# Kernel tuning notes

Measured on AMD Instinct MI355X. Metric: run time of the kernel, lower is better.

## Reference

```python
import jax, jax.numpy as jnp
import numpy as np

B, Z, TDIM, CF, A, R, T = 1024, 256, 512, 1024, 64, 128, 64

def _lstm_cell(x, h, c, Wih, Whh, b):
    # PyTorch gate order: i, f, g, o
    g = x @ Wih.T + h @ Whh.T + b
    i, f, gg, o = jnp.split(g, 4, axis=-1)
    c = jax.nn.sigmoid(f) * c + jax.nn.sigmoid(i) * jnp.tanh(gg)
    h = jax.nn.sigmoid(o) * jnp.tanh(c)
    return h, c

def setup_inputs() -> dict:
    key = jax.random.key(0)
    ks = jax.random.split(key, 24)
    s = lambda k, shape, fan: jax.random.normal(k, shape, jnp.float32) * (1.0 / np.sqrt(fan))
    d = {}
    d['z'] = jax.random.normal(ks[0], (B, Z), jnp.float32)
    d['z2t_w'] = s(ks[1], (TDIM, Z), Z)
    d['z2t_b'] = jnp.zeros((TDIM,), jnp.float32)
    in_a, in_r, in_t = TDIM + A, TDIM + A + R, TDIM + A + 1
    d['Wih_a'] = s(ks[2], (4 * CF, in_a), in_a); d['Whh_a'] = s(ks[3], (4 * CF, CF), CF); d['b_a'] = jnp.zeros((4 * CF,), jnp.float32)
    d['Wih_r'] = s(ks[4], (4 * CF, in_r), in_r); d['Whh_r'] = s(ks[5], (4 * CF, CF), CF); d['b_r'] = jnp.zeros((4 * CF,), jnp.float32)
    d['Wih_t'] = s(ks[6], (4 * CF, in_t), in_t); d['Whh_t'] = s(ks[7], (4 * CF, CF), CF); d['b_t'] = jnp.zeros((4 * CF,), jnp.float32)
    d['e2act_w'] = s(ks[8], (A, CF), CF); d['e2act_b'] = jnp.zeros((A,), jnp.float32)
    d['e2res_w'] = s(ks[9], (R, CF), CF); d['e2res_b'] = jnp.zeros((R,), jnp.float32)
    d['e2ts_w1'] = s(ks[10], (CF // 2, CF), CF); d['e2ts_b1'] = jnp.zeros((CF // 2,), jnp.float32)
    d['e2ts_w2'] = s(ks[11], (1, CF // 2), CF // 2); d['e2ts_b2'] = jnp.zeros((1,), jnp.float32)
    return d

def reference(z, z2t_w, z2t_b, Wih_a, Whh_a, b_a, Wih_r, Whh_r, b_r, Wih_t, Whh_t, b_t,
              e2act_w, e2act_b, e2res_w, e2res_b, e2ts_w1, e2ts_b1, e2ts_w2, e2ts_b2):
    t_rec = jax.nn.relu(z @ z2t_w.T + z2t_b)                  # [B, TDIM]
    b = t_rec.shape[0]
    act_oh = jnp.tile(jax.nn.one_hot(A - 1, A, dtype=jnp.float32), (b, 1))   # EOT activity
    res_oh = jnp.tile(jax.nn.one_hot(R - 1, R, dtype=jnp.float32), (b, 1))   # EOT resource
    ts_v = jnp.zeros((b, 1), jnp.float32)
    zeros_h = jnp.zeros((b, CF), jnp.float32)
    carry0 = (act_oh, res_oh, ts_v, zeros_h, zeros_h, zeros_h, zeros_h, zeros_h, zeros_h)

    def step(carry, _):
        act_oh, res_oh, ts_v, ha, ca, hr, cr, ht, ct = carry
        xa = jnp.concatenate([t_rec, act_oh], axis=-1)
        ha, ca = _lstm_cell(xa, ha, ca, Wih_a, Whh_a, b_a)
        act_logits = ha @ e2act_w.T + e2act_b                 # [B, A]
        act_oh2 = jax.nn.one_hot(jnp.argmax(act_logits, axis=-1), A, dtype=jnp.float32)
        xr = jnp.concatenate([t_rec, act_oh2, res_oh], axis=-1)
        hr, cr = _lstm_cell(xr, hr, cr, Wih_r, Whh_r, b_r)
        res_logits = hr @ e2res_w.T + e2res_b                 # [B, R]
        res_oh2 = jax.nn.one_hot(jnp.argmax(res_logits, axis=-1), R, dtype=jnp.float32)
        xt = jnp.concatenate([t_rec, act_oh2, ts_v], axis=-1)
        ht, ct = _lstm_cell(xt, ht, ct, Wih_t, Whh_t, b_t)
        ts_new = jax.nn.relu(ht @ e2ts_w1.T + e2ts_b1) @ e2ts_w2.T + e2ts_b2  # [B, 1]
        new_carry = (act_oh2, res_oh2, ts_new, ha, ca, hr, cr, ht, ct)
        return new_carry, (act_logits, res_logits, ts_new)

    _, (act_seq, res_seq, ts_seq) = jax.lax.scan(step, carry0, None, length=T)
    acts_rec = jax.nn.softmax(jnp.transpose(act_seq, (1, 0, 2)), axis=2)   # [B, T, A]
    ress_rec = jax.nn.softmax(jnp.transpose(res_seq, (1, 0, 2)), axis=2)   # [B, T, R]
    ts_rec = jnp.transpose(ts_seq[..., 0], (1, 0))                         # [B, T]
    return acts_rec, ts_rec, ress_rec
```

## Files before the change

kernel.cpp:

```cpp
#include <hip/hip_runtime.h>
#include <math.h>


__device__ __forceinline__ float sigf(float x) { return 1.0f / (1.0f + expf(-x)); }

typedef __attribute__((ext_vector_type(8))) _Float16 f16x8;
typedef __attribute__((ext_vector_type(4))) float f32x4;

__device__ __forceinline__ void split_f16(float x, unsigned short& hi, unsigned short& lo) {
    _Float16 h = (_Float16)x;
    float r = (x - (float)h) * 2048.0f;
    _Float16 l = (_Float16)r;
    hi = __builtin_bit_cast(unsigned short, h);
    lo = __builtin_bit_cast(unsigned short, l);
}

#define GLDS(gp, lp) __builtin_amdgcn_global_load_lds( \
    (const __attribute__((address_space(1))) void*)(gp), \
    (__attribute__((address_space(3))) void*)(lp), 16, 0, 0)

__global__ __launch_bounds__(256) void step1(
    const unsigned short* __restrict__ Ah, const unsigned short* __restrict__ Al,
    const unsigned short* __restrict__ WA0, const unsigned short* __restrict__ WA1,
    const float* __restrict__ base_a, const float* __restrict__ Ea, const int* __restrict__ aidx,
    float* __restrict__ ca, unsigned short* __restrict__ oAh, unsigned short* __restrict__ oAl,
    float* __restrict__ haf,
    const unsigned short* __restrict__ Th, const unsigned short* __restrict__ Tl,
    const unsigned short* __restrict__ W10, const unsigned short* __restrict__ W11,
    const float* __restrict__ b1, float* __restrict__ u,
    const float* __restrict__ hrf, const float* __restrict__ resT4, const float* __restrict__ resb,
    float* __restrict__ out_res, int* __restrict__ ridx, int t, int Loff)
{
    int L = blockIdx.x + Loff;
    if (L >= 576) {
        if (t == 0) return;
        int lane = threadIdx.x & 63, w = threadIdx.x >> 6;
        int b = (L - 576) * 4 + w;
        float acc0 = resb[lane], acc1 = resb[lane + 64];
        const float4* arow = (const float4*)(hrf + (size_t)b * 1024);
#pragma unroll 4
        for (int k4 = 0; k4 < 256; k4++) {
            float4 a4 = arow[k4];
            float4 w40 = *(const float4*)(resT4 + ((size_t)k4 * 128 + lane) * 4);
            float4 w41 = *(const float4*)(resT4 + ((size_t)k4 * 128 + lane + 64) * 4);
            acc0 += a4.x * w40.x + a4.y * w40.y + a4.z * w40.z + a4.w * w40.w;
            acc1 += a4.x * w41.x + a4.y * w41.y + a4.z * w41.z + a4.w * w41.w;
        }
        float v = acc0; int idx = lane;
        if (acc1 > v) { v = acc1; idx = lane + 64; }
#pragma unroll
        for (int off = 32; off; off >>= 1) {
            float ov = __shfl_xor(v, off);
            int   oi = __shfl_xor(idx, off);
            if (ov > v || (ov == v && oi < idx)) { v = ov; idx = oi; }
        }
        float e0 = expf(acc0 - v), e1 = expf(acc1 - v);
        float s = e0 + e1;
#pragma unroll
        for (int off = 32; off; off >>= 1) s += __shfl_xor(s, off);
        float* dst = out_res + ((size_t)b * 64 + (t - 1)) * 128;
        dst[lane] = e0 / s; dst[lane + 64] = e1 / s;
        if (lane == 0) ridx[b] = idx;
        return;
    }

    __shared__ unsigned short lds[24576];
    const unsigned short *pAh, *pAl, *pWh, *pWl;
    int x, jy; bool isA;
    if (L < 512) {
        isA = true;
        int xcd = L & 7, idx = L >> 3;
        jy = xcd * 8 + (idx >> 3);
        x = idx & 7;
        pAh = Ah; pAl = Al; pWh = WA0; pWl = WA1;
    } else {
        isA = false;
        int t2 = L - 512;
        x = t2 & 7; jy = t2 >> 3;
        pAh = Th; pAl = Tl; pWh = W10; pWl = W11;
    }
    const int tid = threadIdx.x, wave = tid >> 6, lane = tid & 63;
    const int lrow = lane & 15, lq = lane >> 4;
    const int m0 = x * 128;

    f32x4 acch[2][4], accl[2][4];
#pragma unroll
    for (int i = 0; i < 2; i++)
#pragma unroll
        for (int j = 0; j < 4; j++) {
            acch[i][j] = (f32x4){0.f, 0.f, 0.f, 0.f};
            accl[i][j] = (f32x4){0.f, 0.f, 0.f, 0.f};
        }

    for (int k0 = 0; k0 < 1024; k0 += 64) {
        __syncthreads();
#pragma unroll
        for (int ss = 0; ss < 2; ss++) {
            int s = wave * 2 + ss;
            int mrow = m0 + s * 16 + lrow;
            int nrow = isA ? (wave * 1024 + jy * 16 + lrow) : (jy * 64 + wave * 16 + lrow);
#pragma unroll
            for (int kh = 0; kh < 2; kh++) {
                int k = k0 + kh * 32 + lq * 8;
                GLDS(pAh + (size_t)mrow * 1024 + k, &lds[s * 1024 + kh * 512]);
                GLDS(pAl + (size_t)mrow * 1024 + k, &lds[8192 + s * 1024 + kh * 512]);
                if (ss == 0) {
                    GLDS(pWh + (size_t)nrow * 1024 + k, &lds[16384 + wave * 1024 + kh * 512]);
                    GLDS(pWl + (size_t)nrow * 1024 + k, &lds[20480 + wave * 1024 + kh * 512]);
                }
            }
        }
        __syncthreads();
#pragma unroll
        for (int kh = 0; kh < 2; kh++) {
            f16x8 ah[2], al[2], bh[4], bl[4];
#pragma unroll
            for (int mi = 0; mi < 2; mi++) {
                ah[mi] = *(const f16x8*)&lds[(wave * 2 + mi) * 1024 + kh * 512 + lane * 8];
                al[mi] = *(const f16x8*)&lds[8192 + (wave * 2 + mi) * 1024 + kh * 512 + lane * 8];
            }
#pragma unroll
            for (int ni = 0; ni < 4; ni++) {
                bh[ni] = *(const f16x8*)&lds[16384 + ni * 1024 + kh * 512 + lane * 8];
                bl[ni] = *(const f16x8*)&lds[20480 + ni * 1024 + kh * 512 + lane * 8];
            }
#pragma unroll
            for (int mi = 0; mi < 2; mi++)
#pragma unroll
                for (int ni = 0; ni < 4; ni++) {
                    acch[mi][ni] = __builtin_amdgcn_mfma_f32_16x16x32_f16(ah[mi], bh[ni], acch[mi][ni], 0, 0, 0);
                    accl[mi][ni] = __builtin_amdgcn_mfma_f32_16x16x32_f16(al[mi], bh[ni], accl[mi][ni], 0, 0, 0);
                    accl[mi][ni] = __builtin_amdgcn_mfma_f32_16x16x32_f16(ah[mi], bl[ni], accl[mi][ni], 0, 0, 0);
                }
        }
    }

    const float s_lo = 1.0f / 2048.0f;
    if (isA) {
        int j = jy * 16 + lrow;
#pragma unroll
        for (int mi = 0; mi < 2; mi++)
#pragma unroll
            for (int r = 0; r < 4; r++) {
                int row = m0 + wave * 32 + mi * 16 + lq * 4 + r;
                size_t rb = (size_t)row * 4096 + j;
                const float* e1 = Ea + (size_t)aidx[row] * 4096 + j;
                float gi = acch[mi][0][r] + accl[mi][0][r] * s_lo + base_a[rb]        + e1[0];
                float gf = acch[mi][1][r] + accl[mi][1][r] * s_lo + base_a[rb + 1024] + e1[1024];
                float gg = acch[mi][2][r] + accl[mi][2][r] * s_lo + base_a[rb + 2048] + e1[2048];
                float go = acch[mi][3][r] + accl[mi][3][r] * s_lo + base_a[rb + 3072] + e1[3072];
                size_t ci = (size_t)row * 1024 + j;
                float cn = sigf(gf) * ca[ci] + sigf(gi) * tanhf(gg);
                ca[ci] = cn;
                float hn = sigf(go) * tanhf(cn);
                haf[ci] = hn;
                split_f16(hn, oAh[ci], oAl[ci]);
            }
    } else {
#pragma unroll
        for (int mi = 0; mi < 2; mi++)
#pragma unroll
            for (int ni = 0; ni < 4; ni++) {
                int col = jy * 64 + ni * 16 + lrow;
                float bv = b1[col];
#pragma unroll
                for (int r = 0; r < 4; r++) {
                    int row = m0 + wave * 32 + mi * 16 + lq * 4 + r;
                    float v = acch[mi][ni][r] + accl[mi][ni][r] * s_lo + bv;
                    u[(size_t)row * 512 + col] = fmaxf(v, 0.0f);
                }
            }
    }
}

__global__ __launch_bounds__(256) void step3(
    const unsigned short* __restrict__ Rh, const unsigned short* __restrict__ Rl,
    const unsigned short* __restrict__ WR0, const unsigned short* __restrict__ WR1,
    const float* __restrict__ base_r, const float* __restrict__ Er_a, const float* __restrict__ Er_r,
    const int* __restrict__ aidx, const int* __restrict__ ridx, const float* __restrict__ tsv,
    float* __restrict__ cr, unsigned short* __restrict__ oRh, unsigned short* __restrict__ oRl,
    float* __restrict__ hrf,
    const unsigned short* __restrict__ Th, const unsigned short* __restrict__ Tl,
    const unsigned short* __restrict__ WT0, const unsigned short* __restrict__ WT1,
    const float* __restrict__ base_t, const float* __restrict__ Et_a, const float* __restrict__ wtts,
    float* __restrict__ ct, unsigned short* __restrict__ oTh, unsigned short* __restrict__ oTl)
{
    __shared__ unsigned short lds[32768];
    int L = blockIdx.x;
    int xcd = L & 7, idx = L >> 3;
    int g = xcd * 8 + (idx >> 3);
    int x = idx & 7;
    int z = g >> 5, y = g & 31;
    const unsigned short* pAh = z ? Th : Rh;
    const unsigned short* pAl = z ? Tl : Rl;
    const unsigned short* pWh = z ? WT0 : WR0;
    const unsigned short* pWl = z ? WT1 : WR1;

    const int tid = threadIdx.x, wave = tid >> 6, lane = tid & 63;
    const int wm = wave >> 1, wn = wave & 1;
    const int lrow = lane & 15, lq = lane >> 4;
    const int m0 = x * 128, j0 = y * 32;

    f32x4 acch[4][4], accl[4][4];
#pragma unroll
    for (int i = 0; i < 4; i++)
#pragma unroll
        for (int j = 0; j < 4; j++) {
            acch[i][j] = (f32x4){0.f, 0.f, 0.f, 0.f};
            accl[i][j] = (f32x4){0.f, 0.f, 0.f, 0.f};
        }

    for (int k0 = 0; k0 < 1024; k0 += 64) {
        __syncthreads();
#pragma unroll
        for (int ss = 0; ss < 2; ss++) {
            int s = wave * 2 + ss;
            int mrow = m0 + s * 16 + lrow;
            int nrow = (s >> 1) * 1024 + j0 + (s & 1) * 16 + lrow;
#pragma unroll
            for (int kh = 0; kh < 2; kh++) {
                int k = k0 + kh * 32 + lq * 8;
                GLDS(pAh + (size_t)mrow * 1024 + k, &lds[s * 1024 + kh * 512]);
                GLDS(pAl + (size_t)mrow * 1024 + k, &lds[8192 + s * 1024 + kh * 512]);
                GLDS(pWh + (size_t)nrow * 1024 + k, &lds[16384 + s * 1024 + kh * 512]);
                GLDS(pWl + (size_t)nrow * 1024 + k, &lds[24576 + s * 1024 + kh * 512]);
            }
        }
        __syncthreads();
#pragma unroll
        for (int kh = 0; kh < 2; kh++) {
            f16x8 ah[4], al[4], bh[4], bl[4];
#pragma unroll
            for (int mi = 0; mi < 4; mi++) {
                ah[mi] = *(const f16x8*)&lds[(wm * 4 + mi) * 1024 + kh * 512 + lane * 8];
                al[mi] = *(const f16x8*)&lds[8192 + (wm * 4 + mi) * 1024 + kh * 512 + lane * 8];
            }
#pragma unroll
            for (int ni = 0; ni < 4; ni++) {
                bh[ni] = *(const f16x8*)&lds[16384 + (ni * 2 + wn) * 1024 + kh * 512 + lane * 8];
                bl[ni] = *(const f16x8*)&lds[24576 + (ni * 2 + wn) * 1024 + kh * 512 + lane * 8];
            }
#pragma unroll
            for (int mi = 0; mi < 4; mi++)
#pragma unroll
                for (int ni = 0; ni < 4; ni++) {
                    acch[mi][ni] = __builtin_amdgcn_mfma_f32_16x16x32_f16(ah[mi], bh[ni], acch[mi][ni], 0, 0, 0);
                    accl[mi][ni] = __builtin_amdgcn_mfma_f32_16x16x32_f16(al[mi], bh[ni], accl[mi][ni], 0, 0, 0);
                    accl[mi][ni] = __builtin_amdgcn_mfma_f32_16x16x32_f16(ah[mi], bl[ni], accl[mi][ni], 0, 0, 0);
                }
        }
    }

    const float s_lo = 1.0f / 2048.0f;
    const int j = j0 + wn * 16 + lrow;
    if (z == 0) {
#pragma unroll
        for (int mi = 0; mi < 4; mi++)
#pragma unroll
            for (int r = 0; r < 4; r++) {
                int row = m0 + wm * 64 + mi * 16 + lq * 4 + r;
                size_t rb = (size_t)row * 4096 + j;
                const float* e1 = Er_a + (size_t)aidx[row] * 4096 + j;
                const float* e2 = Er_r + (size_t)ridx[row] * 4096 + j;
                float gi = acch[mi][0][r] + accl[mi][0][r] * s_lo + base_r[rb]        + e1[0]    + e2[0];
                float gf = acch[mi][1][r] + accl[mi][1][r] * s_lo + base_r[rb + 1024] + e1[1024] + e2[1024];
                float gg = acch[mi][2][r] + accl[mi][2][r] * s_lo + base_r[rb + 2048] + e1[2048] + e2[2048];
                float go = acch[mi][3][r] + accl[mi][3][r] * s_lo + base_r[rb + 3072] + e1[3072] + e2[3072];
                size_t ci = (size_t)row * 1024 + j;
                float cn = sigf(gf) * cr[ci] + sigf(gi) * tanhf(gg);
                cr[ci] = cn;
                float hn = sigf(go) * tanhf(cn);
                hrf[ci] = hn;
                split_f16(hn, oRh[ci], oRl[ci]);
            }
    } else {
#pragma unroll
        for (int mi = 0; mi < 4; mi++)
#pragma unroll
            for (int r = 0; r < 4; r++) {
                int row = m0 + wm * 64 + mi * 16 + lq * 4 + r;
                size_t rb = (size_t)row * 4096 + j;
                const float* e1 = Et_a + (size_t)aidx[row] * 4096 + j;
                float tv = tsv[row];
                float gi = acch[mi][0][r] + accl[mi][0][r] * s_lo + base_t[rb]        + e1[0];
                float gf = acch[mi][1][r] + accl[mi][1][r] * s_lo + base_t[rb + 1024] + e1[1024];
                float gg = acch[mi][2][r] + accl[mi][2][r] * s_lo + base_t[rb + 2048] + e1[2048];
                float go = acch[mi][3][r] + accl[mi][3][r] * s_lo + base_t[rb + 3072] + e1[3072];
                gi = fmaf(tv, wtts[j], gi);        gf = fmaf(tv, wtts[j + 1024], gf);
                gg = fmaf(tv, wtts[j + 2048], gg); go = fmaf(tv, wtts[j + 3072], go);
                size_t ci = (size_t)row * 1024 + j;
                float cn = sigf(gf) * ct[ci] + sigf(gi) * tanhf(gg);
                ct[ci] = cn;
                float hn = sigf(go) * tanhf(cn);
                split_f16(hn, oTh[ci], oTl[ci]);
            }
    }
}

__global__ __launch_bounds__(256) void heads(
    const float* __restrict__ haf, const float* __restrict__ actT4, const float* __restrict__ actb,
    float* __restrict__ out_acts, int* __restrict__ aidx, int tact,
    const float* __restrict__ u, const float* __restrict__ w2, const float* __restrict__ b2,
    float* __restrict__ out_ts, float* __restrict__ tsv, int tts)
{
    int blk = blockIdx.x;
    int lane = threadIdx.x & 63, w = threadIdx.x >> 6;
    if (blk < 256) {
        if (tact < 0) return;
        int b = blk * 4 + w;
        float acc = actb[lane];
        const float4* arow = (const float4*)(haf + (size_t)b * 1024);
#pragma unroll 4
        for (int k4 = 0; k4 < 256; k4++) {
            float4 a4 = arow[k4];
            float4 w4 = *(const float4*)(actT4 + ((size_t)k4 * 64 + lane) * 4);
            acc += a4.x * w4.x + a4.y * w4.y + a4.z * w4.z + a4.w * w4.w;
        }
        float v = acc; int idx = lane;
#pragma unroll
        for (int off = 32; off; off >>= 1) {
            float ov = __shfl_xor(v, off);
            int   oi = __shfl_xor(idx, off);
            if (ov > v || (ov == v && oi < idx)) { v = ov; idx = oi; }
        }
        float e = expf(acc - v);
        float s = e;
#pragma unroll
        for (int off = 32; off; off >>= 1) s += __shfl_xor(s, off);
        out_probs_write:
        out_acts[((size_t)b * 64 + tact) * 64 + lane] = e / s;
        if (lane == 0) aidx[b] = idx;
    } else {
        if (tts < 0) return;
        int b = (blk - 256) * 4 + w;
        const float* ur = u + (size_t)b * 512;
        float s = 0.0f;
#pragma unroll
        for (int q = 0; q < 8; q++) s = fmaf(ur[lane + q * 64], w2[lane + q * 64], s);
#pragma unroll
        for (int off = 32; off; off >>= 1) s += __shfl_xor(s, off);
        if (lane == 0) {
            float r = s + b2[0];
            out_ts[b * 64 + tts] = r;
            tsv[b] = r;
        }
    }
}

__global__ __launch_bounds__(256) void gemm_f32(
    const float* __restrict__ A0, const float* __restrict__ W0, float* __restrict__ C0,
    const float* __restrict__ A1, const float* __restrict__ W1, float* __restrict__ C1,
    int lda, int ldw, int ldc, int K, const float* __restrict__ bias, int relu)
{
    const float* Ap = blockIdx.z ? A1 : A0;
    const float* Wp = blockIdx.z ? W1 : W0;
    float*       Cp = blockIdx.z ? C1 : C0;
    __shared__ float As[16][128];
    __shared__ float Bs[16][64];
    const int tid = threadIdx.x;
    const int m0 = blockIdx.x * 128, n0 = blockIdx.y * 64;
    const int tx = tid & 7, ty = tid >> 3;
    const bool wal = (ldw & 3) == 0;
    float acc[4][8];
#pragma unroll
    for (int i = 0; i < 4; i++)
#pragma unroll
        for (int j = 0; j < 8; j++) acc[i][j] = 0.0f;

    for (int k0 = 0; k0 < K; k0 += 16) {
        __syncthreads();
#pragma unroll
        for (int q = 0; q < 2; q++) {
            int t2 = tid + q * 256;
            int kq = t2 & 3, m = t2 >> 2;
            float4 v = *(const float4*)(Ap + (size_t)(m0 + m) * lda + k0 + kq * 4);
            As[kq * 4 + 0][m] = v.x; As[kq * 4 + 1][m] = v.y;
            As[kq * 4 + 2][m] = v.z; As[kq * 4 + 3][m] = v.w;
        }
        {
            int kq = tid & 3, n = tid >> 2;
            const float* src = Wp + (size_t)(n0 + n) * ldw + k0 + kq * 4;
            float4 v;
            if (wal) v = *(const float4*)src;
            else { v.x = src[0]; v.y = src[1]; v.z = src[2]; v.w = src[3]; }
            Bs[kq * 4 + 0][n] = v.x; Bs[kq * 4 + 1][n] = v.y;
            Bs[kq * 4 + 2][n] = v.z; Bs[kq * 4 + 3][n] = v.w;
        }
        __syncthreads();
#pragma unroll
        for (int k = 0; k < 16; k++) {
            float a4[4], b8[8];
            *(float4*)a4 = *(const float4*)&As[k][ty * 4];
            *(float4*)(b8) = *(const float4*)&Bs[k][tx * 8];
            *(float4*)(b8 + 4) = *(const float4*)&Bs[k][tx * 8 + 4];
#pragma unroll
            for (int i = 0; i < 4; i++)
#pragma unroll
                for (int j = 0; j < 8; j++) acc[i][j] = fmaf(a4[i], b8[j], acc[i][j]);
        }
    }
#pragma unroll
    for (int i = 0; i < 4; i++) {
        int m = m0 + ty * 4 + i;
        float vb[8];
#pragma unroll
        for (int j = 0; j < 8; j++) {
            float v = acc[i][j];
            if (bias) v += bias[n0 + tx * 8 + j];
            if (relu) v = fmaxf(v, 0.0f);
            vb[j] = v;
        }
        float* dst = Cp + (size_t)m * ldc + n0 + tx * 8;
        *(float4*)dst = make_float4(vb[0], vb[1], vb[2], vb[3]);
        *(float4*)(dst + 4) = make_float4(vb[4], vb[5], vb[6], vb[7]);
    }
}

__global__ void extract_cols(const float* __restrict__ Wih, int ldw, int col0, int ncols,
                             float* __restrict__ E)
{
    int i = blockIdx.x * 256 + threadIdx.x;
    if (i >= ncols * 4096) return;
    int c = i % ncols, j = i / ncols;
    E[(size_t)c * 4096 + j] = Wih[(size_t)j * ldw + col0 + c];
}

__global__ void split_mat_h(const float* __restrict__ X,
                            unsigned short* __restrict__ hi, unsigned short* __restrict__ lo, int n)
{
    int i = blockIdx.x * 256 + threadIdx.x;
    if (i >= n) return;
    split_f16(X[i], hi[i], lo[i]);
}

__global__ void transpose_pack(const float* __restrict__ W, int K, int C, float* __restrict__ out)
{
    int i = blockIdx.x * 256 + threadIdx.x;
    if (i >= C * K) return;
    int c = i / K, k = i - c * K;
    out[(((size_t)(k >> 2) * C + c) << 2) + (k & 3)] = W[i];
}

__global__ void init_state(float* __restrict__ cc, unsigned int* __restrict__ hilo,
                           float* __restrict__ tsv, int* __restrict__ aidx, int* __restrict__ ridx)
{
    int i = blockIdx.x * 256 + threadIdx.x;
    if (i < 3 * 1024 * 1024) cc[i] = 0.0f;
    if (i < 6 * 1024 * 1024) hilo[i] = 0u;
    if (i < 1024) { tsv[i] = 0.0f; aidx[i] = 63; ridx[i] = 127; }
}

extern "C" void kernel_launch(void* const* d_in, const int* in_sizes, int n_in,
                              void* d_out, int out_size, void* d_ws, size_t ws_size,
                              hipStream_t stream)
{
    const float* z       = (const float*)d_in[0];
    const float* z2t_w   = (const float*)d_in[1];
    const float* z2t_b   = (const float*)d_in[2];
    const float* Wih_a   = (const float*)d_in[3];
    const float* Whh_a   = (const float*)d_in[4];
    const float* b_a     = (const float*)d_in[5];
    const float* Wih_r   = (const float*)d_in[6];
    const float* Whh_r   = (const float*)d_in[7];
    const float* b_r     = (const float*)d_in[8];
    const float* Wih_t   = (const float*)d_in[9];
    const float* Whh_t   = (const float*)d_in[10];
    const float* b_t     = (const float*)d_in[11];
    const float* e2act_w = (const float*)d_in[12];
    const float* e2act_b = (const float*)d_in[13];
    const float* e2res_w = (const float*)d_in[14];
    const float* e2res_b = (const float*)d_in[15];
    const float* e2ts_w1 = (const float*)d_in[16];
    const float* e2ts_b1 = (const float*)d_in[17];
    const float* e2ts_w2 = (const float*)d_in[18];
    const float* e2ts_b2 = (const float*)d_in[19];

    float* out_acts = (float*)d_out;
    float* out_ts   = out_acts + (size_t)1024 * 64 * 64;
    float* out_res  = out_ts + 1024 * 64;

    float* ws = (float*)d_ws;
    size_t off = 0;
    auto alloc = [&](size_t n) { float* p = ws + off; off += n; return p; };
    float* t_rec  = alloc((size_t)1024 * 512);
    float* base_a = alloc((size_t)1024 * 4096);
    float* base_r = alloc((size_t)1024 * 4096);
    float* base_t = alloc((size_t)1024 * 4096);
    float* Ea     = alloc((size_t)64 * 4096);
    float* Er_a   = alloc((size_t)64 * 4096);
    float* Er_r   = alloc((size_t)128 * 4096);
    float* Et_a   = alloc((size_t)64 * 4096);
    float* wtts   = alloc(4096);
    float* cc     = alloc((size_t)3 * 1024 * 1024);
    float* ca = cc, * cr = cc + 1048576, * ct = cc + 2097152;
    float* haf    = alloc((size_t)1024 * 1024);
    float* hrf    = alloc((size_t)1024 * 1024);
    float* u      = alloc((size_t)1024 * 512);
    float* tsv    = alloc(1024);
    int*   aidx   = (int*)alloc(1024);
    int*   ridx   = (int*)alloc(1024);
    float* actT4  = alloc((size_t)64 * 1024);
    float* resT4  = alloc((size_t)128 * 1024);
    unsigned short* hilo = (unsigned short*)alloc((size_t)6 * 1024 * 1024);
    const size_t U = 1048576;
    unsigned short* haSp0[2] = {hilo,         hilo + U};
    unsigned short* haSp1[2] = {hilo + 2 * U, hilo + 3 * U};
    unsigned short* hrSp0[2] = {hilo + 4 * U, hilo + 5 * U};
    unsigned short* hrSp1[2] = {hilo + 6 * U, hilo + 7 * U};
    unsigned short* htSp0[2] = {hilo + 8 * U, hilo + 9 * U};
    unsigned short* htSp1[2] = {hilo + 10 * U, hilo + 11 * U};
    unsigned short* WA0 = (unsigned short*)alloc((size_t)2 * 1024 * 1024);
    unsigned short* WA1 = (unsigned short*)alloc((size_t)2 * 1024 * 1024);
    unsigned short* WR0 = (unsigned short*)alloc((size_t)2 * 1024 * 1024);
    unsigned short* WR1 = (unsigned short*)alloc((size_t)2 * 1024 * 1024);
    unsigned short* WT0 = (unsigned short*)alloc((size_t)2 * 1024 * 1024);
    unsigned short* WT1 = (unsigned short*)alloc((size_t)2 * 1024 * 1024);
    unsigned short* W10 = (unsigned short*)alloc((size_t)256 * 1024);
    unsigned short* W11 = (unsigned short*)alloc((size_t)256 * 1024);

    dim3 blk(256);
    init_state<<<(6 * 1024 * 1024 + 255) / 256, blk, 0, stream>>>(cc, (unsigned int*)hilo, tsv, aidx, ridx);

    gemm_f32<<<dim3(8, 8, 1), blk, 0, stream>>>(z, z2t_w, t_rec, z, z2t_w, t_rec,
                                                256, 256, 512, 256, z2t_b, 1);
    gemm_f32<<<dim3(8, 64, 1), blk, 0, stream>>>(t_rec, Wih_a, base_a, t_rec, Wih_a, base_a,
                                                 512, 576, 4096, 512, b_a, 0);
    gemm_f32<<<dim3(8, 64, 1), blk, 0, stream>>>(t_rec, Wih_r, base_r, t_rec, Wih_r, base_r,
                                                 512, 704, 4096, 512, b_r, 0);
    gemm_f32<<<dim3(8, 64, 1), blk, 0, stream>>>(t_rec, Wih_t, base_t, t_rec, Wih_t, base_t,
                                                 512, 577, 4096, 512, b_t, 0);
    extract_cols<<<(64 * 4096 + 255) / 256, blk, 0, stream>>>(Wih_a, 576, 512, 64, Ea);
    extract_cols<<<(64 * 4096 + 255) / 256, blk, 0, stream>>>(Wih_r, 704, 512, 64, Er_a);
    extract_cols<<<(128 * 4096 + 255) / 256, blk, 0, stream>>>(Wih_r, 704, 576, 128, Er_r);
    extract_cols<<<(64 * 4096 + 255) / 256, blk, 0, stream>>>(Wih_t, 577, 512, 64, Et_a);
    extract_cols<<<(4096 + 255) / 256, blk, 0, stream>>>(Wih_t, 577, 576, 1, wtts);
    transpose_pack<<<(64 * 1024 + 255) / 256, blk, 0, stream>>>(e2act_w, 1024, 64, actT4);
    transpose_pack<<<(128 * 1024 + 255) / 256, blk, 0, stream>>>(e2res_w, 1024, 128, resT4);
    split_mat_h<<<(4194304 + 255) / 256, blk, 0, stream>>>(Whh_a, WA0, WA1, 4194304);
    split_mat_h<<<(4194304 + 255) / 256, blk, 0, stream>>>(Whh_r, WR0, WR1, 4194304);
    split_mat_h<<<(4194304 + 255) / 256, blk, 0, stream>>>(Whh_t, WT0, WT1, 4194304);
    split_mat_h<<<(524288 + 255) / 256, blk, 0, stream>>>(e2ts_w1, W10, W11, 524288);

    for (int t = 0; t < 64; t++) {
        int rd = t & 1, wr = rd ^ 1;
        step1<<<832, blk, 0, stream>>>(
            haSp0[rd], haSp1[rd], WA0, WA1, base_a, Ea, aidx,
            ca, haSp0[wr], haSp1[wr], haf,
            htSp0[rd], htSp1[rd], W10, W11, e2ts_b1, u,
            hrf, resT4, e2res_b, out_res, ridx, t, 0);
        heads<<<512, blk, 0, stream>>>(haf, actT4, e2act_b, out_acts, aidx, t,
                                       u, e2ts_w2, e2ts_b2, out_ts, tsv, t - 1);
        step3<<<512, blk, 0, stream>>>(
            hrSp0[rd], hrSp1[rd], WR0, WR1, base_r, Er_a, Er_r, aidx, ridx, tsv,
            cr, hrSp0[wr], hrSp1[wr], hrf,
            htSp0[rd], htSp1[rd], WT0, WT1, base_t, Et_a, wtts,
            ct, htSp0[wr], htSp1[wr]);
    }
    step1<<<320, blk, 0, stream>>>(
        haSp0[0], haSp1[0], WA0, WA1, base_a, Ea, aidx,
        ca, haSp0[1], haSp1[1], haf,
        htSp0[0], htSp1[0], W10, W11, e2ts_b1, u,
        hrf, resT4, e2res_b, out_res, ridx, 64, 512);
    heads<<<512, blk, 0, stream>>>(haf, actT4, e2act_b, out_acts, aidx, -1,
                                   u, e2ts_w2, e2ts_b2, out_ts, tsv, 63);
}
```

Before: 16.55 ms.

## Double-buffer LDS tiles in LSTM GEMM kernels to overlap loads with MFMA

Both recurrent GEMM kernels switch from a single-buffered K=64 loop with two syncthreads per iteration to a double-buffered K=32 pipeline. The next tile is prefetched with global_load_lds while the current one is computed, and partial vmcnt waits plus raw s_barrier calls control ordering. The aim is to hide global memory latency behind the MFMA work. In exchange there are twice as many iterations and barriers, and correctness now depends on the hand-set vmcnt counts matching the number of outstanding loads per stage.

Measured after the change: 14.71 ms. 11.2% less time.

```diff
diff --git a/kernel.cpp b/kernel.cpp
--- a/kernel.cpp
+++ b/kernel.cpp
@@ -92,48 +92,59 @@
             accl[i][j] = (f32x4){0.f, 0.f, 0.f, 0.f};
         }
 
-    for (int k0 = 0; k0 < 1024; k0 += 64) {
-        __syncthreads();
+    const int nrow = isA ? (wave * 1024 + jy * 16 + lrow) : (jy * 64 + wave * 16 + lrow);
+
+    auto STAGE = [&](int it, int p) {
+        int k = it * 32 + lq * 8;
+        unsigned short* bp = &lds[p * 12288];
 #pragma unroll
         for (int ss = 0; ss < 2; ss++) {
             int s = wave * 2 + ss;
             int mrow = m0 + s * 16 + lrow;
-            int nrow = isA ? (wave * 1024 + jy * 16 + lrow) : (jy * 64 + wave * 16 + lrow);
-#pragma unroll
-            for (int kh = 0; kh < 2; kh++) {
-                int k = k0 + kh * 32 + lq * 8;
-                GLDS(pAh + (size_t)mrow * 1024 + k, &lds[s * 1024 + kh * 512]);
-                GLDS(pAl + (size_t)mrow * 1024 + k, &lds[8192 + s * 1024 + kh * 512]);
-                if (ss == 0) {
-                    GLDS(pWh + (size_t)nrow * 1024 + k, &lds[16384 + wave * 1024 + kh * 512]);
-                    GLDS(pWl + (size_t)nrow * 1024 + k, &lds[20480 + wave * 1024 + kh * 512]);
-                }
+            GLDS(pAh + (size_t)mrow * 1024 + k, bp + s * 512);
+            GLDS(pAl + (size_t)mrow * 1024 + k, bp + 4096 + s * 512);
+        }
+        GLDS(pWh + (size_t)nrow * 1024 + k, bp + 8192 + wave * 512);
+        GLDS(pWl + (size_t)nrow * 1024 + k, bp + 10240 + wave * 512);
+    };
+    auto COMPUTE = [&](int p) {
+        unsigned short* bp = &lds[p * 12288];
+        f16x8 ah[2], al[2], bh[4], bl[4];
+#pragma unroll
+        for (int mi = 0; mi < 2; mi++) {
+            ah[mi] = *(const f16x8*)(bp + (wave * 2 + mi) * 512 + lane * 8);
+            al[mi] = *(const f16x8*)(bp + 4096 + (wave * 2 + mi) * 512 + lane * 8);
+        }
+#pragma unroll
+        for (int ni = 0; ni < 4; ni++) {
+            bh[ni] = *(const f16x8*)(bp + 8192 + ni * 512 + lane * 8);
+            bl[ni] = *(const f16x8*)(bp + 10240 + ni * 512 + lane * 8);
+        }
+#pragma unroll
+        for (int mi = 0; mi < 2; mi++)
+#pragma unroll
+            for (int ni = 0; ni < 4; ni++) {
+                acch[mi][ni] = __builtin_amdgcn_mfma_f32_16x16x32_f16(ah[mi], bh[ni], acch[mi][ni], 0, 0, 0);
+                accl[mi][ni] = __builtin_amdgcn_mfma_f32_16x16x32_f16(al[mi], bh[ni], accl[mi][ni], 0, 0, 0);
+                accl[mi][ni] = __builtin_amdgcn_mfma_f32_16x16x32_f16(ah[mi], bl[ni], accl[mi][ni], 0, 0, 0);
             }
-        }
-        __syncthreads();
-#pragma unroll
-        for (int kh = 0; kh < 2; kh++) {
-            f16x8 ah[2], al[2], bh[4], bl[4];
-#pragma unroll
-            for (int mi = 0; mi < 2; mi++) {
-                ah[mi] = *(const f16x8*)&lds[(wave * 2 + mi) * 1024 + kh * 512 + lane * 8];
-                al[mi] = *(const f16x8*)&lds[8192 + (wave * 2 + mi) * 1024 + kh * 512 + lane * 8];
-            }
-#pragma unroll
-            for (int ni = 0; ni < 4; ni++) {
-                bh[ni] = *(const f16x8*)&lds[16384 + ni * 1024 + kh * 512 + lane * 8];
-                bl[ni] = *(const f16x8*)&lds[20480 + ni * 1024 + kh * 512 + lane * 8];
-            }
-#pragma unroll
-            for (int mi = 0; mi < 2; mi++)
-#pragma unroll
-                for (int ni = 0; ni < 4; ni++) {
-                    acch[mi][ni] = __builtin_amdgcn_mfma_f32_16x16x32_f16(ah[mi], bh[ni], acch[mi][ni], 0, 0, 0);
-                    accl[mi][ni] = __builtin_amdgcn_mfma_f32_16x16x32_f16(al[mi], bh[ni], accl[mi][ni], 0, 0, 0);
-                    accl[mi][ni] = __builtin_amdgcn_mfma_f32_16x16x32_f16(ah[mi], bl[ni], accl[mi][ni], 0, 0, 0);
-                }
-        }
-    }
+    };
+
+    STAGE(0, 0);
+    for (int it = 0; it < 31; ++it) {
+        int cur = it & 1;
+        STAGE(it + 1, cur ^ 1);
+        asm volatile("s_waitcnt vmcnt(6)" ::: "memory");
+        __builtin_amdgcn_s_barrier();
+        __builtin_amdgcn_sched_barrier(0);
+        COMPUTE(cur);
+        __builtin_amdgcn_sched_barrier(0);
+        __builtin_amdgcn_s_barrier();
+    }
+    asm volatile("s_waitcnt vmcnt(0)" ::: "memory");
+    __builtin_amdgcn_s_barrier();
+    __builtin_amdgcn_sched_barrier(0);
+    COMPUTE(1);
 
     const float s_lo = 1.0f / 2048.0f;
     if (isA) {
@@ -210,46 +221,58 @@
             accl[i][j] = (f32x4){0.f, 0.f, 0.f, 0.f};
         }
 
-    for (int k0 = 0; k0 < 1024; k0 += 64) {
-        __syncthreads();
+    auto STAGE = [&](int it, int p) {
+        int k = it * 32 + lq * 8;
+        unsigned short* bp = &lds[p * 16384];
 #pragma unroll
         for (int ss = 0; ss < 2; ss++) {
             int s = wave * 2 + ss;
             int mrow = m0 + s * 16 + lrow;
             int nrow = (s >> 1) * 1024 + j0 + (s & 1) * 16 + lrow;
-#pragma unroll
-            for (int kh = 0; kh < 2; kh++) {
-                int k = k0 + kh * 32 + lq * 8;
-                GLDS(pAh + (size_t)mrow * 1024 + k, &lds[s * 1024 + kh * 512]);
-                GLDS(pAl + (size_t)mrow * 1024 + k, &lds[8192 + s * 1024 + kh * 512]);
-                GLDS(pWh + (size_t)nrow * 1024 + k, &lds[16384 + s * 1024 + kh * 512]);
-                GLDS(pWl + (size_t)nrow * 1024 + k, &lds[24576 + s * 1024 + kh * 512]);
+            GLDS(pAh + (size_t)mrow * 1024 + k, bp + s * 512);
+            GLDS(pAl + (size_t)mrow * 1024 + k, bp + 4096 + s * 512);
+            GLDS(pWh + (size_t)nrow * 1024 + k, bp + 8192 + s * 512);
+            GLDS(pWl + (size_t)nrow * 1024 + k, bp + 12288 + s * 512);
+        }
+    };
+    auto COMPUTE = [&](int p) {
+        unsigned short* bp = &lds[p * 16384];
+        f16x8 ah[4], al[4], bh[4], bl[4];
+#pragma unroll
+        for (int mi = 0; mi < 4; mi++) {
+            ah[mi] = *(const f16x8*)(bp + (wm * 4 + mi) * 512 + lane * 8);
+            al[mi] = *(const f16x8*)(bp + 4096 + (wm * 4 + mi) * 512 + lane * 8);
+        }
+#pragma unroll
+        for (int ni = 0; ni < 4; ni++) {
+            bh[ni] = *(const f16x8*)(bp + 8192 + (ni * 2 + wn) * 512 + lane * 8);
+            bl[ni] = *(const f16x8*)(bp + 12288 + (ni * 2 + wn) * 512 + lane * 8);
+        }
+#pragma unroll
+        for (int mi = 0; mi < 4; mi++)
+#pragma unroll
+            for (int ni = 0; ni < 4; ni++) {
+                acch[mi][ni] = __builtin_amdgcn_mfma_f32_16x16x32_f16(ah[mi], bh[ni], acch[mi][ni], 0, 0, 0);
+                accl[mi][ni] = __builtin_amdgcn_mfma_f32_16x16x32_f16(al[mi], bh[ni], accl[mi][ni], 0, 0, 0);
+                accl[mi][ni] = __builtin_amdgcn_mfma_f32_16x16x32_f16(ah[mi], bl[ni], accl[mi][ni], 0, 0, 0);
             }
-        }
-        __syncthreads();
-#pragma unroll
-        for (int kh = 0; kh < 2; kh++) {
-            f16x8 ah[4], al[4], bh[4], bl[4];
-#pragma unroll
-            for (int mi = 0; mi < 4; mi++) {
-                ah[mi] = *(const f16x8*)&lds[(wm * 4 + mi) * 1024 + kh * 512 + lane * 8];
-                al[mi] = *(const f16x8*)&lds[8192 + (wm * 4 + mi) * 1024 + kh * 512 + lane * 8];
-            }
-#pragma unroll
-            for (int ni = 0; ni < 4; ni++) {
-                bh[ni] = *(const f16x8*)&lds[16384 + (ni * 2 + wn) * 1024 + kh * 512 + lane * 8];
-                bl[ni] = *(const f16x8*)&lds[24576 + (ni * 2 + wn) * 1024 + kh * 512 + lane * 8];
-            }
-#pragma unroll
-            for (int mi = 0; mi < 4; mi++)
-#pragma unroll
-                for (int ni = 0; ni < 4; ni++) {
-                    acch[mi][ni] = __builtin_amdgcn_mfma_f32_16x16x32_f16(ah[mi], bh[ni], acch[mi][ni], 0, 0, 0);
-                    accl[mi][ni] = __builtin_amdgcn_mfma_f32_16x16x32_f16(al[mi], bh[ni], accl[mi][ni], 0, 0, 0);
-                    accl[mi][ni] = __builtin_amdgcn_mfma_f32_16x16x32_f16(ah[mi], bl[ni], accl[mi][ni], 0, 0, 0);
-                }
-        }
-    }
+    };
+
+    STAGE(0, 0);
+    for (int it = 0; it < 31; ++it) {
+        int cur = it & 1;
+        STAGE(it + 1, cur ^ 1);
+        asm volatile("s_waitcnt vmcnt(8)" ::: "memory");
+        __builtin_amdgcn_s_barrier();
+        __builtin_amdgcn_sched_barrier(0);
+        COMPUTE(cur);
+        __builtin_amdgcn_sched_barrier(0);
+        __builtin_amdgcn_s_barrier();
+    }
+    asm volatile("s_waitcnt vmcnt(0)" ::: "memory");
+    __builtin_amdgcn_s_barrier();
+    __builtin_amdgcn_sched_barrier(0);
+    COMPUTE(1);
 
     const float s_lo = 1.0f / 2048.0f;
     const int j = j0 + wn * 16 + lrow;
@@ -327,7 +350,6 @@
         float s = e;
 #pragma unroll
         for (int off = 32; off; off >>= 1) s += __shfl_xor(s, off);
-        out_probs_write:
         out_acts[((size_t)b * 64 + tact) * 64 + lane] = e / s;
         if (lane == 0) aidx[b] = idx;
     } else {
```
